# Kernel tuning notes

Hardware: AMD Instinct MI355X
Metric: run time of the kernel (lower is better)

## Reference

```python
import jax, jax.numpy as jnp
import numpy as np

B, M, D = 2048, 40, 16
LAYERS = [128, 128, 128]


def setup_inputs() -> dict:
    key = jax.random.key(0)
    ks = jax.random.split(key, 8)
    s = 0.05
    x = jax.random.normal(ks[0], (B, M, D), jnp.float32)
    w0 = jax.random.normal(ks[1], (128, M * M), jnp.float32) * s      # in = n_dim*n_dim = 1600
    b0 = jax.random.normal(ks[2], (128,), jnp.float32) * s
    w1 = jax.random.normal(ks[3], (128, 64 * M), jnp.float32) * s     # prev halved to 64 -> in = 2560
    b1 = jax.random.normal(ks[4], (128,), jnp.float32) * s
    w2 = jax.random.normal(ks[5], (128, 64 * M), jnp.float32) * s
    b2 = jax.random.normal(ks[6], (128,), jnp.float32) * s
    wl = jax.random.normal(ks[7], (1, 64 * 3), jnp.float32) * s       # n_feat_map = 64+64+64
    return {"x": x, "w0": w0, "b0": b0, "w1": w1, "b1": b1,
            "w2": w2, "b2": b2, "wl": wl}


def reference(x, w0, b0, w1, b1, w2, b2, wl):
    # x: [B, M, D]; CIN with half_split=True and all-even layers.
    _, m, _ = x.shape
    prev = x
    direct = []
    for w, b in ((w0, b0), (w1, b1), (w2, b2)):
        h = prev.shape[1]
        o = w.shape[0]
        wr = w.reshape(o, h, m)
        # Fused outer-product + 1x1 conv:
        # einsum('bhd,bmd->bhmd') reshaped to [B, h*m, D] then conv1d(k=1)
        out = jnp.einsum('bhd,bmd,ohm->bod', prev, x, wr) + b[None, :, None]
        out = jax.nn.relu(out)
        half = o // 2
        prev = out[:, :half]          # next hidden
        direct.append(out[:, half:])  # direct connection
    feat = jnp.concatenate(direct, axis=1).sum(-1)  # [B, n_feat_map]
    return feat @ wl.T  # [B, 1]
```

## Files before the change

### kernel.cpp

```cpp
#include <hip/hip_runtime.h>
#include <hip/hip_bf16.h>

typedef short bf16x8 __attribute__((ext_vector_type(8)));
typedef float f32x4  __attribute__((ext_vector_type(4)));

__device__ __forceinline__ unsigned cvt2(float a, float b) {
  __hip_bfloat162 h = __float22bfloat162_rn(make_float2(a, b));
  unsigned u; __builtin_memcpy(&u, &h, 4); return u;
}

__device__ __forceinline__ f32x4 MFMA(bf16x8 a, bf16x8 b, f32x4 c) {
  return __builtin_amdgcn_mfma_f32_16x16x32_bf16(a, b, c, 0, 0, 0);
}

__device__ __forceinline__ int xp_idx(int n, int h) { return (n << 6) + (h ^ ((n & 15) << 2)); }

__global__ __launch_bounds__(256) void permute_w_kernel(
    const float* __restrict__ w0, const float* __restrict__ w1,
    const float* __restrict__ w2, unsigned short* __restrict__ Wp) {
  __shared__ float rowt[40 * 65];
  const int b = blockIdx.x;
  const float* src; unsigned short* dst; int K, LZ;
  if (b < 128)      { src = w0 + b * 1600;            dst = Wp + b * 1600;            K = 1600; LZ = 1; }
  else if (b < 256) { int o = b - 128; src = w1 + o * 2560; dst = Wp + 204800 + o * 2560; K = 2560; LZ = 0; }
  else              { int o = b - 256; src = w2 + o * 2560; dst = Wp + 532480 + o * 2560; K = 2560; LZ = 0; }
  for (int i = threadIdx.x; i < (K >> 2); i += 256) {
    float4 v = ((const float4*)src)[i];
    int f = i << 2;
    int h = f / 40, m = f - h * 40;
    rowt[(m + 0) * 65 + h] = v.x;
    rowt[(m + 1) * 65 + h] = v.y;
    rowt[(m + 2) * 65 + h] = v.z;
    rowt[(m + 3) * 65 + h] = v.w;
  }
  __syncthreads();
  for (int i = threadIdx.x; i < (K >> 3); i += 256) {
    const int k = i << 3;
    int m, h;
    if (LZ) { m = k / 40; h = k - m * 40; } else { m = k >> 6; h = k & 63; }
    const float* p = &rowt[m * 65 + h];
    uint4 u;
    u.x = cvt2(p[0], p[1]); u.y = cvt2(p[2], p[3]);
    u.z = cvt2(p[4], p[5]); u.w = cvt2(p[6], p[7]);
    *(uint4*)&dst[k] = u;
  }
}

__global__ __launch_bounds__(512, 2) void cin_kernel(
    const float* __restrict__ x, const unsigned short* __restrict__ Wp,
    const float* __restrict__ bias0, const float* __restrict__ bias1,
    const float* __restrict__ bias2, const float* __restrict__ wl,
    float* __restrict__ out) {
  __shared__ __align__(16) float XP_s[128 * 64];
  __shared__ __align__(16) float XT_s[40 * 128];
  __shared__ __align__(16) float scr_s[4 * 4096];
  __shared__ float wl_s[192];
  __shared__ float s_s[128];

  const int tid = threadIdx.x;
  const int lane = tid & 63;
  const int wv = tid >> 6;
  const int bid = blockIdx.x;

  if (tid < 192) wl_s[tid] = wl[tid];
  if (tid < 128) s_s[tid] = 0.f;

  {
    const float4* xg = (const float4*)(x + (size_t)bid * 5120);
    for (int i = tid; i < 1280; i += 512) {
      float4 v = xg[i];
      int d4 = (i & 3) << 2;
      int m = (i >> 2) % 40;
      int b_l = i / 160;
      int nb = b_l * 16 + d4;
      XP_s[xp_idx(nb + 0, m)] = v.x;
      XP_s[xp_idx(nb + 1, m)] = v.y;
      XP_s[xp_idx(nb + 2, m)] = v.z;
      XP_s[xp_idx(nb + 3, m)] = v.w;
      *(float4*)&XT_s[(m << 7) + nb] = v;
    }
  }

  const int nlo = lane & 15;
  const int q = lane >> 4;
  const int orow = q << 2;
  const int swn = nlo << 2;

  auto mkB = [&](const f32x4& pa, const f32x4& pb, float xv) -> bf16x8 {
    uint4 u;
    u.x = cvt2(pa[0] * xv, pa[1] * xv);
    u.y = cvt2(pa[2] * xv, pa[3] * xv);
    u.z = cvt2(pb[0] * xv, pb[1] * xv);
    u.w = cvt2(pb[2] * xv, pb[3] * xv);
    return __builtin_bit_cast(bf16x8, u);
  };

  __syncthreads();

  {
    const int ohalf = wv & 1, khalf = (wv >> 1) & 1, nhalf = wv >> 2;
    const int obase = ohalf << 6;
    const int nf0 = (nhalf << 6) + nlo;
    const int k0 = (khalf << 5) + (q << 3);

    f32x4 acc[4][4];
#pragma unroll
    for (int a = 0; a < 4; ++a)
#pragma unroll
      for (int b = 0; b < 4; ++b) acc[a][b] = f32x4{0.f, 0.f, 0.f, 0.f};

    const unsigned short* wp[4];
#pragma unroll
    for (int mr = 0; mr < 4; ++mr)
      wp[mr] = Wp + (size_t)(obase + mr * 16 + nlo) * 1600 + k0;

    int m = (k0 >= 40) ? 1 : 0;
    int h = k0 - 40 * m;

    bf16x8 Aa[4], Ab[4];
#pragma unroll
    for (int mr = 0; mr < 4; ++mr) Aa[mr] = *(const bf16x8*)(wp[mr]);

    auto stepL0 = [&](bf16x8 (&A)[4]) {
#pragma unroll
      for (int fn = 0; fn < 4; ++fn) {
        const int nf = nf0 + fn * 16;
        const int rb = nf << 6;
        f32x4 pa = *(const f32x4*)&XP_s[rb + (h ^ swn)];
        f32x4 pb = *(const f32x4*)&XP_s[rb + ((h + 4) ^ swn)];
        float xv = XT_s[(m << 7) + nf];
        bf16x8 B = mkB(pa, pb, xv);
#pragma unroll
        for (int mr = 0; mr < 4; ++mr) acc[mr][fn] = MFMA(A[mr], B, acc[mr][fn]);
      }
      h += 24; ++m;
      if (h >= 40) { h -= 40; ++m; }
    };

    for (int s = 0; s < 24; s += 2) {
#pragma unroll
      for (int mr = 0; mr < 4; ++mr) Ab[mr] = *(const bf16x8*)(wp[mr] + (s + 1) * 64);
      stepL0(Aa);
#pragma unroll
      for (int mr = 0; mr < 4; ++mr) Aa[mr] = *(const bf16x8*)(wp[mr] + (s + 2) * 64);
      stepL0(Ab);
    }
    stepL0(Aa);

    const int pid = (nhalf << 1) | ohalf;
    __syncthreads();
    if (khalf == 1) {
#pragma unroll
      for (int mr = 0; mr < 4; ++mr)
#pragma unroll
        for (int fn = 0; fn < 4; ++fn)
          *(f32x4*)&scr_s[pid * 4096 + (mr * 4 + fn) * 256 + lane * 4] = acc[mr][fn];
    }
    __syncthreads();
    if (khalf == 0) {
#pragma unroll
      for (int mr = 0; mr < 4; ++mr)
#pragma unroll
        for (int fn = 0; fn < 4; ++fn)
          acc[mr][fn] += *(const f32x4*)&scr_s[pid * 4096 + (mr * 4 + fn) * 256 + lane * 4];
      if (ohalf == 0) {
#pragma unroll
        for (int mr = 0; mr < 4; ++mr) {
          const int o0 = mr * 16 + orow;
          float4 bv = *(const float4*)&bias0[o0];
#pragma unroll
          for (int fn = 0; fn < 4; ++fn) {
            f32x4 a = acc[mr][fn];
            float4 r;
            r.x = fmaxf(a[0] + bv.x, 0.f);
            r.y = fmaxf(a[1] + bv.y, 0.f);
            r.z = fmaxf(a[2] + bv.z, 0.f);
            r.w = fmaxf(a[3] + bv.w, 0.f);
            *(float4*)&XP_s[xp_idx(nf0 + fn * 16, o0)] = r;
          }
        }
      } else {
        float dir[4] = {0.f, 0.f, 0.f, 0.f};
#pragma unroll
        for (int mr = 0; mr < 4; ++mr) {
          const int o0 = 64 + mr * 16 + orow;
          float4 bv = *(const float4*)&bias0[o0];
          float4 wv4 = *(const float4*)&wl_s[o0 - 64];
#pragma unroll
          for (int fn = 0; fn < 4; ++fn) {
            f32x4 a = acc[mr][fn];
            dir[fn] += fmaxf(a[0] + bv.x, 0.f) * wv4.x
                     + fmaxf(a[1] + bv.y, 0.f) * wv4.y
                     + fmaxf(a[2] + bv.z, 0.f) * wv4.z
                     + fmaxf(a[3] + bv.w, 0.f) * wv4.w;
          }
        }
#pragma unroll
        for (int fn = 0; fn < 4; ++fn) {
          float v = dir[fn];
          v += __shfl_xor(v, 16);
          v += __shfl_xor(v, 32);
          if (lane < 16) atomicAdd(&s_s[(nhalf << 6) + fn * 16 + lane], v);
        }
      }
    }
    __syncthreads();
  }

  for (int lidx = 1; lidx < 3; ++lidx) {
    const unsigned short* W = (lidx == 1) ? (Wp + 204800) : (Wp + 532480);
    const float* bias = (lidx == 1) ? bias1 : bias2;
    const int oq = wv >> 1, khalf = wv & 1;
    const int obase = oq << 5;
    const int h0 = (khalf << 5) + (q << 3);

    f32x4 Pc[8][2];
#pragma unroll
    for (int fn = 0; fn < 8; ++fn) {
      const int rb = (fn * 16 + nlo) << 6;
      Pc[fn][0] = *(const f32x4*)&XP_s[rb + (h0 ^ swn)];
      Pc[fn][1] = *(const f32x4*)&XP_s[rb + ((h0 + 4) ^ swn)];
    }

    f32x4 acc[2][8];
#pragma unroll
    for (int a = 0; a < 2; ++a)
#pragma unroll
      for (int b = 0; b < 8; ++b) acc[a][b] = f32x4{0.f, 0.f, 0.f, 0.f};

    const unsigned short* wp[2];
#pragma unroll
    for (int mr = 0; mr < 2; ++mr)
      wp[mr] = W + (size_t)(obase + mr * 16 + nlo) * 2560 + h0;

    bf16x8 Aa[2], Ab[2];
#pragma unroll
    for (int mr = 0; mr < 2; ++mr) Aa[mr] = *(const bf16x8*)(wp[mr]);

    for (int s = 0; s < 40; s += 2) {
#pragma unroll
      for (int mr = 0; mr < 2; ++mr) Ab[mr] = *(const bf16x8*)(wp[mr] + 64);
#pragma unroll
      for (int fn = 0; fn < 8; ++fn) {
        float xv = XT_s[(s << 7) + fn * 16 + nlo];
        bf16x8 B = mkB(Pc[fn][0], Pc[fn][1], xv);
        acc[0][fn] = MFMA(Aa[0], B, acc[0][fn]);
        acc[1][fn] = MFMA(Aa[1], B, acc[1][fn]);
      }
      const int offn = (s + 2 < 40) ? 128 : 64;
#pragma unroll
      for (int mr = 0; mr < 2; ++mr) Aa[mr] = *(const bf16x8*)(wp[mr] + offn);
#pragma unroll
      for (int fn = 0; fn < 8; ++fn) {
        float xv = XT_s[((s + 1) << 7) + fn * 16 + nlo];
        bf16x8 B = mkB(Pc[fn][0], Pc[fn][1], xv);
        acc[0][fn] = MFMA(Ab[0], B, acc[0][fn]);
        acc[1][fn] = MFMA(Ab[1], B, acc[1][fn]);
      }
      wp[0] += 128; wp[1] += 128;
    }

    __syncthreads();
    if (khalf == 1) {
#pragma unroll
      for (int mr = 0; mr < 2; ++mr)
#pragma unroll
        for (int fn = 0; fn < 8; ++fn)
          *(f32x4*)&scr_s[oq * 4096 + (mr * 8 + fn) * 256 + lane * 4] = acc[mr][fn];
    }
    __syncthreads();
    if (khalf == 0) {
#pragma unroll
      for (int mr = 0; mr < 2; ++mr)
#pragma unroll
        for (int fn = 0; fn < 8; ++fn)
          acc[mr][fn] += *(const f32x4*)&scr_s[oq * 4096 + (mr * 8 + fn) * 256 + lane * 4];
      if (oq < 2) {
        if (lidx < 2) {
#pragma unroll
          for (int mr = 0; mr < 2; ++mr) {
            const int o0 = obase + mr * 16 + orow;
            float4 bv = *(const float4*)&bias[o0];
#pragma unroll
            for (int fn = 0; fn < 8; ++fn) {
              f32x4 a = acc[mr][fn];
              float4 r;
              r.x = fmaxf(a[0] + bv.x, 0.f);
              r.y = fmaxf(a[1] + bv.y, 0.f);
              r.z = fmaxf(a[2] + bv.z, 0.f);
              r.w = fmaxf(a[3] + bv.w, 0.f);
              *(float4*)&XP_s[xp_idx(fn * 16 + nlo, o0)] = r;
            }
          }
        }
      } else {
        float dir[8] = {0.f, 0.f, 0.f, 0.f, 0.f, 0.f, 0.f, 0.f};
#pragma unroll
        for (int mr = 0; mr < 2; ++mr) {
          const int o0 = 64 + (oq - 2) * 32 + mr * 16 + orow;
          float4 bv = *(const float4*)&bias[o0];
          float4 wv4 = *(const float4*)&wl_s[lidx * 64 + (o0 - 64)];
#pragma unroll
          for (int fn = 0; fn < 8; ++fn) {
            f32x4 a = acc[mr][fn];
            dir[fn] += fmaxf(a[0] + bv.x, 0.f) * wv4.x
                     + fmaxf(a[1] + bv.y, 0.f) * wv4.y
                     + fmaxf(a[2] + bv.z, 0.f) * wv4.z
                     + fmaxf(a[3] + bv.w, 0.f) * wv4.w;
          }
        }
#pragma unroll
        for (int fn = 0; fn < 8; ++fn) {
          float v = dir[fn];
          v += __shfl_xor(v, 16);
          v += __shfl_xor(v, 32);
          if (lane < 16) atomicAdd(&s_s[fn * 16 + lane], v);
        }
      }
    }
    __syncthreads();
  }

  if (tid < 8) {
    float s = 0.f;
#pragma unroll
    for (int d = 0; d < 16; ++d) s += s_s[tid * 16 + d];
    out[bid * 8 + tid] = s;
  }
}

extern "C" void kernel_launch(void* const* d_in, const int* in_sizes, int n_in,
                              void* d_out, int out_size, void* d_ws, size_t ws_size,
                              hipStream_t stream) {
  const float* x  = (const float*)d_in[0];
  const float* w0 = (const float*)d_in[1];
  const float* b0 = (const float*)d_in[2];
  const float* w1 = (const float*)d_in[3];
  const float* b1 = (const float*)d_in[4];
  const float* w2 = (const float*)d_in[5];
  const float* b2 = (const float*)d_in[6];
  const float* wl = (const float*)d_in[7];
  unsigned short* Wp = (unsigned short*)d_ws;

  permute_w_kernel<<<384, 256, 0, stream>>>(w0, w1, w2, Wp);
  cin_kernel<<<256, 512, 0, stream>>>(x, Wp, b0, b1, b2, wl, (float*)d_out);
}
```

Baseline: 160.5 us.

## Unify CIN layers with zero-padded layer-0 weights and per-wave full-O tiling

Layer 0's weight rows are padded from 1600 to 2560 with zeros, and the unused hidden slots 40..63 in the activation tile are zeroed. This lets all three layers share one loop. Work is re-split so each wave computes all 128 outputs for 32 batch-feature columns over half of the M range, with three-deep register prefetch of weight fragments. The direct-connection reduction is kept in registers across layers and written once, replacing per-layer shared atomics. This trades about 60% extra MFMA work in layer 0 for simpler code, better reuse of the B operand, and fewer atomics, at the cost of higher register pressure from the A0/A1/A2 arrays.

```diff
diff --git a/kernel.cpp b/kernel.cpp
--- a/kernel.cpp
+++ b/kernel.cpp
@@ -20,11 +20,11 @@
     const float* __restrict__ w2, unsigned short* __restrict__ Wp) {
   __shared__ float rowt[40 * 65];
   const int b = blockIdx.x;
-  const float* src; unsigned short* dst; int K, LZ;
-  if (b < 128)      { src = w0 + b * 1600;            dst = Wp + b * 1600;            K = 1600; LZ = 1; }
-  else if (b < 256) { int o = b - 128; src = w1 + o * 2560; dst = Wp + 204800 + o * 2560; K = 2560; LZ = 0; }
-  else              { int o = b - 256; src = w2 + o * 2560; dst = Wp + 532480 + o * 2560; K = 2560; LZ = 0; }
-  for (int i = threadIdx.x; i < (K >> 2); i += 256) {
+  const float* src; unsigned short* dst; int Kin, L0;
+  if (b < 128)      { src = w0 + b * 1600;            dst = Wp + (size_t)b * 2560;            Kin = 1600; L0 = 1; }
+  else if (b < 256) { int o = b - 128; src = w1 + o * 2560; dst = Wp + 327680 + (size_t)o * 2560; Kin = 2560; L0 = 0; }
+  else              { int o = b - 256; src = w2 + o * 2560; dst = Wp + 655360 + (size_t)o * 2560; Kin = 2560; L0 = 0; }
+  for (int i = threadIdx.x; i < (Kin >> 2); i += 256) {
     float4 v = ((const float4*)src)[i];
     int f = i << 2;
     int h = f / 40, m = f - h * 40;
@@ -34,15 +34,18 @@
     rowt[(m + 3) * 65 + h] = v.w;
   }
   __syncthreads();
-  for (int i = threadIdx.x; i < (K >> 3); i += 256) {
+  for (int i = threadIdx.x; i < 320; i += 256) {
     const int k = i << 3;
-    int m, h;
-    if (LZ) { m = k / 40; h = k - m * 40; } else { m = k >> 6; h = k & 63; }
-    const float* p = &rowt[m * 65 + h];
-    uint4 u;
-    u.x = cvt2(p[0], p[1]); u.y = cvt2(p[2], p[3]);
-    u.z = cvt2(p[4], p[5]); u.w = cvt2(p[6], p[7]);
-    *(uint4*)&dst[k] = u;
+    const int m = k >> 6, h = k & 63;
+    if (L0 && h >= 40) {
+      *(uint4*)&dst[k] = make_uint4(0u, 0u, 0u, 0u);
+    } else {
+      const float* p = &rowt[m * 65 + h];
+      uint4 u;
+      u.x = cvt2(p[0], p[1]); u.y = cvt2(p[2], p[3]);
+      u.z = cvt2(p[4], p[5]); u.w = cvt2(p[6], p[7]);
+      *(uint4*)&dst[k] = u;
+    }
   }
 }
 
@@ -63,7 +66,6 @@
   const int bid = blockIdx.x;
 
   if (tid < 192) wl_s[tid] = wl[tid];
-  if (tid < 128) s_s[tid] = 0.f;
 
   {
     const float4* xg = (const float4*)(x + (size_t)bid * 5120);
@@ -79,248 +81,170 @@
       XP_s[xp_idx(nb + 3, m)] = v.w;
       *(float4*)&XT_s[(m << 7) + nb] = v;
     }
+    for (int i = tid; i < 768; i += 512) {
+      int n = i / 6, hg = 40 + (i - n * 6) * 4;
+      *(float4*)&XP_s[xp_idx(n, hg)] = make_float4(0.f, 0.f, 0.f, 0.f);
+    }
   }
 
   const int nlo = lane & 15;
   const int q = lane >> 4;
   const int orow = q << 2;
   const int swn = nlo << 2;
-
-  auto mkB = [&](const f32x4& pa, const f32x4& pb, float xv) -> bf16x8 {
+  const int khalf = wv & 1;
+  const int nq = wv >> 1;
+  const int n0 = nq * 32 + nlo;
+  const int kb0 = khalf * 1280;
+  const int mbase = khalf * 20;
+  const int hq0 = q << 3;
+  const int hq1 = 32 + (q << 3);
+
+  auto mkB = [&](const f32x4& lo, const f32x4& hi, float xv) -> bf16x8 {
     uint4 u;
-    u.x = cvt2(pa[0] * xv, pa[1] * xv);
-    u.y = cvt2(pa[2] * xv, pa[3] * xv);
-    u.z = cvt2(pb[0] * xv, pb[1] * xv);
-    u.w = cvt2(pb[2] * xv, pb[3] * xv);
+    u.x = cvt2(lo[0] * xv, lo[1] * xv);
+    u.y = cvt2(lo[2] * xv, lo[3] * xv);
+    u.z = cvt2(hi[0] * xv, hi[1] * xv);
+    u.w = cvt2(hi[2] * xv, hi[3] * xv);
     return __builtin_bit_cast(bf16x8, u);
   };
 
+  float sacc[2] = {0.f, 0.f};
+
   __syncthreads();
 
-  {
-    const int ohalf = wv & 1, khalf = (wv >> 1) & 1, nhalf = wv >> 2;
-    const int obase = ohalf << 6;
-    const int nf0 = (nhalf << 6) + nlo;
-    const int k0 = (khalf << 5) + (q << 3);
-
-    f32x4 acc[4][4];
-#pragma unroll
-    for (int a = 0; a < 4; ++a)
-#pragma unroll
-      for (int b = 0; b < 4; ++b) acc[a][b] = f32x4{0.f, 0.f, 0.f, 0.f};
-
-    const unsigned short* wp[4];
-#pragma unroll
-    for (int mr = 0; mr < 4; ++mr)
-      wp[mr] = Wp + (size_t)(obase + mr * 16 + nlo) * 1600 + k0;
-
-    int m = (k0 >= 40) ? 1 : 0;
-    int h = k0 - 40 * m;
-
-    bf16x8 Aa[4], Ab[4];
-#pragma unroll
-    for (int mr = 0; mr < 4; ++mr) Aa[mr] = *(const bf16x8*)(wp[mr]);
-
-    auto stepL0 = [&](bf16x8 (&A)[4]) {
-#pragma unroll
-      for (int fn = 0; fn < 4; ++fn) {
-        const int nf = nf0 + fn * 16;
-        const int rb = nf << 6;
-        f32x4 pa = *(const f32x4*)&XP_s[rb + (h ^ swn)];
-        f32x4 pb = *(const f32x4*)&XP_s[rb + ((h + 4) ^ swn)];
-        float xv = XT_s[(m << 7) + nf];
-        bf16x8 B = mkB(pa, pb, xv);
-#pragma unroll
-        for (int mr = 0; mr < 4; ++mr) acc[mr][fn] = MFMA(A[mr], B, acc[mr][fn]);
-      }
-      h += 24; ++m;
-      if (h >= 40) { h -= 40; ++m; }
-    };
-
-    for (int s = 0; s < 24; s += 2) {
-#pragma unroll
-      for (int mr = 0; mr < 4; ++mr) Ab[mr] = *(const bf16x8*)(wp[mr] + (s + 1) * 64);
-      stepL0(Aa);
-#pragma unroll
-      for (int mr = 0; mr < 4; ++mr) Aa[mr] = *(const bf16x8*)(wp[mr] + (s + 2) * 64);
-      stepL0(Ab);
-    }
-    stepL0(Aa);
-
-    const int pid = (nhalf << 1) | ohalf;
+  const float* biasL[3] = {bias0, bias1, bias2};
+
+  for (int lidx = 0; lidx < 3; ++lidx) {
+    const unsigned short* W = Wp + lidx * 327680;
+    const float* bias = biasL[lidx];
+
+    const int rb0 = n0 << 6;
+    const int rb1 = (n0 + 16) << 6;
+    f32x4 Pc00a = *(const f32x4*)&XP_s[rb0 + (hq0 ^ swn)];
+    f32x4 Pc00b = *(const f32x4*)&XP_s[rb0 + ((hq0 + 4) ^ swn)];
+    f32x4 Pc01a = *(const f32x4*)&XP_s[rb0 + (hq1 ^ swn)];
+    f32x4 Pc01b = *(const f32x4*)&XP_s[rb0 + ((hq1 + 4) ^ swn)];
+    f32x4 Pc10a = *(const f32x4*)&XP_s[rb1 + (hq0 ^ swn)];
+    f32x4 Pc10b = *(const f32x4*)&XP_s[rb1 + ((hq0 + 4) ^ swn)];
+    f32x4 Pc11a = *(const f32x4*)&XP_s[rb1 + (hq1 ^ swn)];
+    f32x4 Pc11b = *(const f32x4*)&XP_s[rb1 + ((hq1 + 4) ^ swn)];
+
+    f32x4 acc[8][2];
+#pragma unroll
+    for (int a = 0; a < 8; ++a) { acc[a][0] = f32x4{0.f,0.f,0.f,0.f}; acc[a][1] = f32x4{0.f,0.f,0.f,0.f}; }
+
+    const unsigned short* wr[8];
+#pragma unroll
+    for (int mr = 0; mr < 8; ++mr)
+      wr[mr] = W + (size_t)(mr * 16 + nlo) * 2560 + kb0 + (q << 3);
+
+    bf16x8 A0[8], A1[8], A2[8];
+#pragma unroll
+    for (int mr = 0; mr < 8; ++mr) A0[mr] = *(const bf16x8*)(wr[mr]);
+
+    for (int mi = 0; mi < 20; mi += 2) {
+      const int t0 = mi << 1;
+#pragma unroll
+      for (int mr = 0; mr < 8; ++mr) A1[mr] = *(const bf16x8*)(wr[mr] + (t0 + 1) * 32);
+      float xv0 = XT_s[((mbase + mi) << 7) + n0];
+      float xv1 = XT_s[((mbase + mi) << 7) + n0 + 16];
+      bf16x8 B0 = mkB(Pc00a, Pc00b, xv0);
+      bf16x8 B1 = mkB(Pc10a, Pc10b, xv1);
+#pragma unroll
+      for (int mr = 0; mr < 8; ++mr) A2[mr] = *(const bf16x8*)(wr[mr] + (t0 + 2) * 32);
+#pragma unroll
+      for (int mr = 0; mr < 8; ++mr) {
+        acc[mr][0] = MFMA(A0[mr], B0, acc[mr][0]);
+        acc[mr][1] = MFMA(A0[mr], B1, acc[mr][1]);
+      }
+      B0 = mkB(Pc01a, Pc01b, xv0);
+      B1 = mkB(Pc11a, Pc11b, xv1);
+#pragma unroll
+      for (int mr = 0; mr < 8; ++mr) {
+        acc[mr][0] = MFMA(A1[mr], B0, acc[mr][0]);
+        acc[mr][1] = MFMA(A1[mr], B1, acc[mr][1]);
+      }
+#pragma unroll
+      for (int mr = 0; mr < 8; ++mr) A1[mr] = *(const bf16x8*)(wr[mr] + (t0 + 3) * 32);
+      xv0 = XT_s[((mbase + mi + 1) << 7) + n0];
+      xv1 = XT_s[((mbase + mi + 1) << 7) + n0 + 16];
+      B0 = mkB(Pc00a, Pc00b, xv0);
+      B1 = mkB(Pc10a, Pc10b, xv1);
+      const int t4 = (mi + 2 < 20) ? (t0 + 4) : 0;
+#pragma unroll
+      for (int mr = 0; mr < 8; ++mr) A0[mr] = *(const bf16x8*)(wr[mr] + t4 * 32);
+#pragma unroll
+      for (int mr = 0; mr < 8; ++mr) {
+        acc[mr][0] = MFMA(A2[mr], B0, acc[mr][0]);
+        acc[mr][1] = MFMA(A2[mr], B1, acc[mr][1]);
+      }
+      B0 = mkB(Pc01a, Pc01b, xv0);
+      B1 = mkB(Pc11a, Pc11b, xv1);
+#pragma unroll
+      for (int mr = 0; mr < 8; ++mr) {
+        acc[mr][0] = MFMA(A1[mr], B0, acc[mr][0]);
+        acc[mr][1] = MFMA(A1[mr], B1, acc[mr][1]);
+      }
+    }
+
     __syncthreads();
     if (khalf == 1) {
 #pragma unroll
-      for (int mr = 0; mr < 4; ++mr)
-#pragma unroll
-        for (int fn = 0; fn < 4; ++fn)
-          *(f32x4*)&scr_s[pid * 4096 + (mr * 4 + fn) * 256 + lane * 4] = acc[mr][fn];
+      for (int mr = 0; mr < 8; ++mr)
+#pragma unroll
+        for (int fn = 0; fn < 2; ++fn)
+          *(f32x4*)&scr_s[nq * 4096 + (mr * 2 + fn) * 256 + lane * 4] = acc[mr][fn];
     }
     __syncthreads();
     if (khalf == 0) {
 #pragma unroll
-      for (int mr = 0; mr < 4; ++mr)
-#pragma unroll
-        for (int fn = 0; fn < 4; ++fn)
-          acc[mr][fn] += *(const f32x4*)&scr_s[pid * 4096 + (mr * 4 + fn) * 256 + lane * 4];
-      if (ohalf == 0) {
+      for (int mr = 0; mr < 8; ++mr)
+#pragma unroll
+        for (int fn = 0; fn < 2; ++fn)
+          acc[mr][fn] += *(const f32x4*)&scr_s[nq * 4096 + (mr * 2 + fn) * 256 + lane * 4];
+      if (lidx < 2) {
 #pragma unroll
         for (int mr = 0; mr < 4; ++mr) {
           const int o0 = mr * 16 + orow;
-          float4 bv = *(const float4*)&bias0[o0];
-#pragma unroll
-          for (int fn = 0; fn < 4; ++fn) {
+          float4 bv = *(const float4*)&bias[o0];
+#pragma unroll
+          for (int fn = 0; fn < 2; ++fn) {
             f32x4 a = acc[mr][fn];
             float4 r;
             r.x = fmaxf(a[0] + bv.x, 0.f);
             r.y = fmaxf(a[1] + bv.y, 0.f);
             r.z = fmaxf(a[2] + bv.z, 0.f);
             r.w = fmaxf(a[3] + bv.w, 0.f);
-            *(float4*)&XP_s[xp_idx(nf0 + fn * 16, o0)] = r;
+            *(float4*)&XP_s[xp_idx(n0 + fn * 16, o0)] = r;
           }
         }
-      } else {
-        float dir[4] = {0.f, 0.f, 0.f, 0.f};
-#pragma unroll
-        for (int mr = 0; mr < 4; ++mr) {
-          const int o0 = 64 + mr * 16 + orow;
-          float4 bv = *(const float4*)&bias0[o0];
-          float4 wv4 = *(const float4*)&wl_s[o0 - 64];
-#pragma unroll
-          for (int fn = 0; fn < 4; ++fn) {
-            f32x4 a = acc[mr][fn];
-            dir[fn] += fmaxf(a[0] + bv.x, 0.f) * wv4.x
-                     + fmaxf(a[1] + bv.y, 0.f) * wv4.y
-                     + fmaxf(a[2] + bv.z, 0.f) * wv4.z
-                     + fmaxf(a[3] + bv.w, 0.f) * wv4.w;
-          }
+      }
+#pragma unroll
+      for (int mr = 4; mr < 8; ++mr) {
+        const int o0 = mr * 16 + orow;
+        float4 bv = *(const float4*)&bias[o0];
+        float4 wv4 = *(const float4*)&wl_s[lidx * 64 + (o0 - 64)];
+#pragma unroll
+        for (int fn = 0; fn < 2; ++fn) {
+          f32x4 a = acc[mr][fn];
+          sacc[fn] += fmaxf(a[0] + bv.x, 0.f) * wv4.x
+                    + fmaxf(a[1] + bv.y, 0.f) * wv4.y
+                    + fmaxf(a[2] + bv.z, 0.f) * wv4.z
+                    + fmaxf(a[3] + bv.w, 0.f) * wv4.w;
         }
-#pragma unroll
-        for (int fn = 0; fn < 4; ++fn) {
-          float v = dir[fn];
-          v += __shfl_xor(v, 16);
-          v += __shfl_xor(v, 32);
-          if (lane < 16) atomicAdd(&s_s[(nhalf << 6) + fn * 16 + lane], v);
-        }
       }
     }
     __syncthreads();
   }
 
-  for (int lidx = 1; lidx < 3; ++lidx) {
-    const unsigned short* W = (lidx == 1) ? (Wp + 204800) : (Wp + 532480);
-    const float* bias = (lidx == 1) ? bias1 : bias2;
-    const int oq = wv >> 1, khalf = wv & 1;
-    const int obase = oq << 5;
-    const int h0 = (khalf << 5) + (q << 3);
-
-    f32x4 Pc[8][2];
-#pragma unroll
-    for (int fn = 0; fn < 8; ++fn) {
-      const int rb = (fn * 16 + nlo) << 6;
-      Pc[fn][0] = *(const f32x4*)&XP_s[rb + (h0 ^ swn)];
-      Pc[fn][1] = *(const f32x4*)&XP_s[rb + ((h0 + 4) ^ swn)];
-    }
-
-    f32x4 acc[2][8];
-#pragma unroll
-    for (int a = 0; a < 2; ++a)
-#pragma unroll
-      for (int b = 0; b < 8; ++b) acc[a][b] = f32x4{0.f, 0.f, 0.f, 0.f};
-
-    const unsigned short* wp[2];
-#pragma unroll
-    for (int mr = 0; mr < 2; ++mr)
-      wp[mr] = W + (size_t)(obase + mr * 16 + nlo) * 2560 + h0;
-
-    bf16x8 Aa[2], Ab[2];
-#pragma unroll
-    for (int mr = 0; mr < 2; ++mr) Aa[mr] = *(const bf16x8*)(wp[mr]);
-
-    for (int s = 0; s < 40; s += 2) {
-#pragma unroll
-      for (int mr = 0; mr < 2; ++mr) Ab[mr] = *(const bf16x8*)(wp[mr] + 64);
-#pragma unroll
-      for (int fn = 0; fn < 8; ++fn) {
-        float xv = XT_s[(s << 7) + fn * 16 + nlo];
-        bf16x8 B = mkB(Pc[fn][0], Pc[fn][1], xv);
-        acc[0][fn] = MFMA(Aa[0], B, acc[0][fn]);
-        acc[1][fn] = MFMA(Aa[1], B, acc[1][fn]);
-      }
-      const int offn = (s + 2 < 40) ? 128 : 64;
-#pragma unroll
-      for (int mr = 0; mr < 2; ++mr) Aa[mr] = *(const bf16x8*)(wp[mr] + offn);
-#pragma unroll
-      for (int fn = 0; fn < 8; ++fn) {
-        float xv = XT_s[((s + 1) << 7) + fn * 16 + nlo];
-        bf16x8 B = mkB(Pc[fn][0], Pc[fn][1], xv);
-        acc[0][fn] = MFMA(Ab[0], B, acc[0][fn]);
-        acc[1][fn] = MFMA(Ab[1], B, acc[1][fn]);
-      }
-      wp[0] += 128; wp[1] += 128;
-    }
-
-    __syncthreads();
-    if (khalf == 1) {
-#pragma unroll
-      for (int mr = 0; mr < 2; ++mr)
-#pragma unroll
-        for (int fn = 0; fn < 8; ++fn)
-          *(f32x4*)&scr_s[oq * 4096 + (mr * 8 + fn) * 256 + lane * 4] = acc[mr][fn];
-    }
-    __syncthreads();
-    if (khalf == 0) {
-#pragma unroll
-      for (int mr = 0; mr < 2; ++mr)
-#pragma unroll
-        for (int fn = 0; fn < 8; ++fn)
-          acc[mr][fn] += *(const f32x4*)&scr_s[oq * 4096 + (mr * 8 + fn) * 256 + lane * 4];
-      if (oq < 2) {
-        if (lidx < 2) {
-#pragma unroll
-          for (int mr = 0; mr < 2; ++mr) {
-            const int o0 = obase + mr * 16 + orow;
-            float4 bv = *(const float4*)&bias[o0];
-#pragma unroll
-            for (int fn = 0; fn < 8; ++fn) {
-              f32x4 a = acc[mr][fn];
-              float4 r;
-              r.x = fmaxf(a[0] + bv.x, 0.f);
-              r.y = fmaxf(a[1] + bv.y, 0.f);
-              r.z = fmaxf(a[2] + bv.z, 0.f);
-              r.w = fmaxf(a[3] + bv.w, 0.f);
-              *(float4*)&XP_s[xp_idx(fn * 16 + nlo, o0)] = r;
-            }
-          }
-        }
-      } else {
-        float dir[8] = {0.f, 0.f, 0.f, 0.f, 0.f, 0.f, 0.f, 0.f};
-#pragma unroll
-        for (int mr = 0; mr < 2; ++mr) {
-          const int o0 = 64 + (oq - 2) * 32 + mr * 16 + orow;
-          float4 bv = *(const float4*)&bias[o0];
-          float4 wv4 = *(const float4*)&wl_s[lidx * 64 + (o0 - 64)];
-#pragma unroll
-          for (int fn = 0; fn < 8; ++fn) {
-            f32x4 a = acc[mr][fn];
-            dir[fn] += fmaxf(a[0] + bv.x, 0.f) * wv4.x
-                     + fmaxf(a[1] + bv.y, 0.f) * wv4.y
-                     + fmaxf(a[2] + bv.z, 0.f) * wv4.z
-                     + fmaxf(a[3] + bv.w, 0.f) * wv4.w;
-          }
-        }
-#pragma unroll
-        for (int fn = 0; fn < 8; ++fn) {
-          float v = dir[fn];
-          v += __shfl_xor(v, 16);
-          v += __shfl_xor(v, 32);
-          if (lane < 16) atomicAdd(&s_s[fn * 16 + lane], v);
-        }
-      }
-    }
-    __syncthreads();
-  }
-
+#pragma unroll
+  for (int fn = 0; fn < 2; ++fn) {
+    float v = sacc[fn];
+    v += __shfl_xor(v, 16);
+    v += __shfl_xor(v, 32);
+    if (khalf == 0 && lane < 16) s_s[nq * 32 + fn * 16 + lane] = v;
+  }
+  __syncthreads();
   if (tid < 8) {
     float s = 0.f;
 #pragma unroll
```

Result: slower. 290.1 us (+80.7%).
